# Kernel optimization log

Hardware: AMD Instinct MI355X
Metric: run time of the kernel (lower is better)

## Reference

```python
import jax, jax.numpy as jnp
import numpy as np

ATTN = 512
HIDDEN = 1024
NUM_GENES = 2048
NUM_GF = 4


def setup_inputs() -> dict:
    key = jax.random.key(0)
    ks = jax.random.split(key, 8)
    s = 0.1
    return {
        "genes": jax.random.normal(ks[0], (32, NUM_GENES, NUM_GF), dtype=jnp.float32),
        "smiles": jax.random.normal(ks[1], (32, 2048, HIDDEN), dtype=jnp.float32),
        "w_num_gene_features": s * jax.random.normal(ks[2], (NUM_GF,), dtype=jnp.float32),
        "w_genes": s * jax.random.normal(ks[3], (NUM_GENES, ATTN), dtype=jnp.float32),
        "b_genes": s * jax.random.normal(ks[4], (ATTN,), dtype=jnp.float32),
        "w_smiles": s * jax.random.normal(ks[5], (HIDDEN, ATTN), dtype=jnp.float32),
        "b_smiles": s * jax.random.normal(ks[6], (ATTN,), dtype=jnp.float32),
        "v": s * jax.random.normal(ks[7], (ATTN,), dtype=jnp.float32),
    }


def reference(genes, smiles, w_num_gene_features, w_genes, b_genes, w_smiles, b_smiles, v):
    # genes: [B, G, F] -> collapse feature axis: [B, G]
    genes_collapsed = jnp.einsum("bgf,f->bg", genes, w_num_gene_features)
    # gene context projection: [B, A]
    x = jnp.einsum("bg,ga->ba", genes_collapsed, w_genes) + b_genes
    # smiles projection: [B, T, A]
    y = jnp.einsum("bth,ha->bta", smiles, w_smiles) + b_smiles
    h = jnp.tanh(x[:, None, :] + y)  # [B, T, A]
    scores = jnp.einsum("bta,a->bt", h, v)  # [B, T]
    alphas = jax.nn.softmax(scores, axis=-1)  # [B, T]
    # attention-weighted sum over sequence: [B, H]
    return jnp.einsum("bth,bt->bh", smiles, alphas)
```

## Files before the change

kernel.cpp:

```cpp
#include <hip/hip_runtime.h>


typedef __bf16 bf16_t;
typedef bf16_t bf16x8 __attribute__((ext_vector_type(8)));
typedef float f32x4 __attribute__((ext_vector_type(4)));

__device__ __forceinline__ unsigned short f32_to_bf16_rne(float f) {
    unsigned int u = __builtin_bit_cast(unsigned int, f);
    u = (u + 0x7FFFu + ((u >> 16) & 1u)) >> 16;
    return (unsigned short)u;
}

__device__ __forceinline__ float fast_tanh(float x) {
    float cx = fminf(fmaxf(x, -30.f), 30.f);
    float e = __expf(2.f * cx);
    return (e - 1.f) / (e + 1.f);
}

__global__ void k0b_pack(const float* __restrict__ w, unsigned short* __restrict__ Bp) {
    int bid  = blockIdx.x;
    int lane = threadIdx.x;
    int atile = bid >> 5, gks = bid & 31;
    int col = atile * 16 + (lane & 15);
    int k0  = gks * 32 + (lane >> 4) * 8;
    unsigned short us[8];
#pragma unroll
    for (int e = 0; e < 8; ++e)
        us[e] = f32_to_bf16_rne(w[(size_t)(k0 + e) * 512 + col]);
    *(uint4*)(Bp + (size_t)bid * 512 + lane * 8) = *(const uint4*)us;
}

__global__ void k1a_gc(const float4* __restrict__ genes, const float* __restrict__ wngf,
                       float* __restrict__ gc) {
    int i = blockIdx.x * 256 + threadIdx.x;
    float4 g = genes[i];
    gc[i] = g.x * wngf[0] + g.y * wngf[1] + g.z * wngf[2] + g.w * wngf[3];
}

__global__ void k1b_x(const float* __restrict__ gc, const float* __restrict__ wg,
                      float* __restrict__ x) {
    __shared__ float gcl[256];
    int bx = blockIdx.x;
    int b = bx >> 4, ah = (bx >> 3) & 1, gch = bx & 7;
    int g0 = gch * 256;
    gcl[threadIdx.x] = gc[b * 2048 + g0 + threadIdx.x];
    __syncthreads();
    int a = ah * 256 + threadIdx.x;
    float s = 0.f;
#pragma unroll 8
    for (int g = 0; g < 256; ++g) s += gcl[g] * wg[(size_t)(g0 + g) * 512 + a];
    atomicAdd(&x[b * 512 + a], s);
}

__global__ __launch_bounds__(512, 4) void k2_scores(
    const float* __restrict__ smiles,
    const unsigned short* __restrict__ Bp,
    const float* __restrict__ xraw,
    const float* __restrict__ b_genes,
    const float* __restrict__ b_smiles,
    const float* __restrict__ v,
    float* __restrict__ scores)
{
    __shared__ unsigned short A_lds[2 * 64 * 128];
    __shared__ float score_lds[64];
    const int tid  = threadIdx.x;
    const int wave = tid >> 6;
    const int lane = tid & 63;
    const int l15  = lane & 15;
    const int l4   = lane >> 4;
    const int gm0  = blockIdx.x * 64;
    const int bidx = gm0 >> 11;
    const int wbase = wave * 64;

    const unsigned short* bpp = Bp + (size_t)(wave * 128) * 512 + lane * 8;

    const int srow = tid >> 3;
    const float* sptr = smiles + (size_t)(gm0 + srow) * 1024 + (tid & 7) * 16;
    const int sswz = (srow & 7) << 4;
    char* wr0 = (char*)A_lds + srow * 256 + (((tid & 7) * 32) ^ sswz);
    char* wr1 = (char*)A_lds + srow * 256 + ((((tid & 7) * 32) + 16) ^ sswz);

    if (tid < 64) score_lds[tid] = 0.f;

    float4 st0, st1, st2, st3;

    const f32x4 zero4 = {0.f, 0.f, 0.f, 0.f};
    f32x4 acc[4][4];
#pragma unroll
    for (int mt = 0; mt < 4; ++mt)
#pragma unroll
        for (int nt = 0; nt < 4; ++nt)
            acc[mt][nt] = zero4;

#define LOADREGS(kt)                                   \
    {   const float* p = sptr + (kt) * 128;            \
        st0 = *(const float4*)(p);                     \
        st1 = *(const float4*)(p + 4);                 \
        st2 = *(const float4*)(p + 8);                 \
        st3 = *(const float4*)(p + 12); }

#define CONVWRITE(buf)                                                     \
    {   union { unsigned short us[8]; uint4 u4; } pa, pb;                  \
        pa.us[0] = f32_to_bf16_rne(st0.x); pa.us[1] = f32_to_bf16_rne(st0.y); \
        pa.us[2] = f32_to_bf16_rne(st0.z); pa.us[3] = f32_to_bf16_rne(st0.w); \
        pa.us[4] = f32_to_bf16_rne(st1.x); pa.us[5] = f32_to_bf16_rne(st1.y); \
        pa.us[6] = f32_to_bf16_rne(st1.z); pa.us[7] = f32_to_bf16_rne(st1.w); \
        pb.us[0] = f32_to_bf16_rne(st2.x); pb.us[1] = f32_to_bf16_rne(st2.y); \
        pb.us[2] = f32_to_bf16_rne(st2.z); pb.us[3] = f32_to_bf16_rne(st2.w); \
        pb.us[4] = f32_to_bf16_rne(st3.x); pb.us[5] = f32_to_bf16_rne(st3.y); \
        pb.us[6] = f32_to_bf16_rne(st3.z); pb.us[7] = f32_to_bf16_rne(st3.w); \
        *(uint4*)(wr0 + (buf) * 16384) = pa.u4;                            \
        *(uint4*)(wr1 + (buf) * 16384) = pb.u4; }

#define COMPUTE(cur, kt)                                                      \
    _Pragma("unroll")                                                         \
    for (int ks4 = 0; ks4 < 4; ++ks4) {                                       \
        int gks = (kt) * 4 + ks4;                                             \
        bf16x8 af[4], bfb[4];                                                 \
        _Pragma("unroll")                                                     \
        for (int nt = 0; nt < 4; ++nt)                                        \
            bfb[nt] = *(const bf16x8*)(bpp + (nt * 32 + gks) * 512);          \
        _Pragma("unroll")                                                     \
        for (int mt = 0; mt < 4; ++mt) {                                      \
            int row = mt * 16 + l15;                                          \
            int byteoff = (cur) * 16384 + row * 256 +                         \
                          ((ks4 * 64 + l4 * 16) ^ ((row & 7) << 4));          \
            af[mt] = *(const bf16x8*)((const char*)A_lds + byteoff);          \
        }                                                                     \
        __builtin_amdgcn_s_setprio(1);                                        \
        _Pragma("unroll")                                                     \
        for (int mt = 0; mt < 4; ++mt)                                        \
            _Pragma("unroll")                                                 \
            for (int nt = 0; nt < 4; ++nt)                                    \
                acc[mt][nt] = __builtin_amdgcn_mfma_f32_16x16x32_bf16(        \
                    af[mt], bfb[nt], acc[mt][nt], 0, 0, 0);                   \
        __builtin_amdgcn_s_setprio(0);                                        \
    }

    LOADREGS(0);
    CONVWRITE(0);
    __syncthreads();

    int cur = 0;
#pragma unroll 1
    for (int kt = 0; kt < 7; ++kt) {
        LOADREGS(kt + 1);
        COMPUTE(cur, kt);
        CONVWRITE(cur ^ 1);
        __syncthreads();
        cur ^= 1;
    }
    COMPUTE(cur, 7);

#undef LOADREGS
#undef CONVWRITE
#undef COMPUTE

    float xbv[4], vv[4];
#pragma unroll
    for (int nt = 0; nt < 4; ++nt) {
        int a = wbase + nt * 16 + l15;
        xbv[nt] = xraw[bidx * 512 + a] + b_genes[a] + b_smiles[a];
        vv[nt]  = v[a];
    }
    float rs[4][4];
#pragma unroll
    for (int mt = 0; mt < 4; ++mt)
#pragma unroll
        for (int r = 0; r < 4; ++r)
            rs[mt][r] = 0.f;
#pragma unroll
    for (int mt = 0; mt < 4; ++mt)
#pragma unroll
        for (int nt = 0; nt < 4; ++nt)
#pragma unroll
            for (int r = 0; r < 4; ++r)
                rs[mt][r] += vv[nt] * fast_tanh(acc[mt][nt][r] + xbv[nt]);
#pragma unroll
    for (int mt = 0; mt < 4; ++mt)
#pragma unroll
        for (int r = 0; r < 4; ++r) {
            float s = rs[mt][r];
            s += __shfl_xor(s, 1);
            s += __shfl_xor(s, 2);
            s += __shfl_xor(s, 4);
            s += __shfl_xor(s, 8);
            rs[mt][r] = s;
        }
    if (l15 == 0) {
#pragma unroll
        for (int mt = 0; mt < 4; ++mt)
#pragma unroll
            for (int r = 0; r < 4; ++r)
                atomicAdd(&score_lds[mt * 16 + l4 * 4 + r], rs[mt][r]);
    }
    __syncthreads();
    if (tid < 64) scores[gm0 + tid] = score_lds[tid];
}

__global__ void k4_soft(const float* __restrict__ smiles,
                        const float* __restrict__ scores,
                        float* __restrict__ out)
{
    __shared__ float redmax[4], redsum[4], al_lds[64];
    int bx = blockIdx.x;
    int b  = bx >> 5;
    int tc = bx & 31;
    int tid = threadIdx.x;
    int wid = tid >> 6;

    float sv[8];
    float mx = -1e30f;
#pragma unroll
    for (int i = 0; i < 8; ++i) {
        sv[i] = scores[b * 2048 + i * 256 + tid];
        mx = fmaxf(mx, sv[i]);
    }
#pragma unroll
    for (int m = 32; m >= 1; m >>= 1) mx = fmaxf(mx, __shfl_xor(mx, m));
    if ((tid & 63) == 0) redmax[wid] = mx;
    __syncthreads();
    mx = fmaxf(fmaxf(redmax[0], redmax[1]), fmaxf(redmax[2], redmax[3]));
    float zp = 0.f;
#pragma unroll
    for (int i = 0; i < 8; ++i) zp += __expf(sv[i] - mx);
#pragma unroll
    for (int m = 32; m >= 1; m >>= 1) zp += __shfl_xor(zp, m);
    if ((tid & 63) == 0) redsum[wid] = zp;
    __syncthreads();
    float invZ = 1.f / (redsum[0] + redsum[1] + redsum[2] + redsum[3]);
    if (tid < 64)
        al_lds[tid] = __expf(scores[b * 2048 + tc * 64 + tid] - mx) * invZ;
    __syncthreads();

    int h = tid * 4;
    const float* sb = smiles + ((size_t)b * 2048 + tc * 64) * 1024;
    float4 acc = {0.f, 0.f, 0.f, 0.f};
#pragma unroll 4
    for (int t = 0; t < 64; ++t) {
        float a = al_lds[t];
        float4 sv4 = *(const float4*)(sb + (size_t)t * 1024 + h);
        acc.x += a * sv4.x;
        acc.y += a * sv4.y;
        acc.z += a * sv4.z;
        acc.w += a * sv4.w;
    }
    float* o = out + b * 1024 + h;
    atomicAdd(o + 0, acc.x);
    atomicAdd(o + 1, acc.y);
    atomicAdd(o + 2, acc.z);
    atomicAdd(o + 3, acc.w);
}

extern "C" void kernel_launch(void* const* d_in, const int* in_sizes, int n_in,
                              void* d_out, int out_size, void* d_ws, size_t ws_size,
                              hipStream_t stream) {
    const float* genes    = (const float*)d_in[0];
    const float* smiles   = (const float*)d_in[1];
    const float* w_ngf    = (const float*)d_in[2];
    const float* w_genes  = (const float*)d_in[3];
    const float* b_genes  = (const float*)d_in[4];
    const float* w_smiles = (const float*)d_in[5];
    const float* b_smiles = (const float*)d_in[6];
    const float* v        = (const float*)d_in[7];
    float* out = (float*)d_out;

    char* ws = (char*)d_ws;
    unsigned short* Bp = (unsigned short*)(ws);
    float* gc     = (float*)(ws + (1 << 20));
    float* x      = (float*)(ws + (1 << 20) + (256 << 10));
    float* scores = (float*)(ws + (1 << 20) + (320 << 10));

    hipMemsetAsync(out, 0, (size_t)32 * 1024 * sizeof(float), stream);
    hipMemsetAsync(x, 0, (size_t)64 * 1024, stream);

    k0b_pack<<<1024, 64, 0, stream>>>(w_smiles, Bp);
    k1a_gc<<<256, 256, 0, stream>>>((const float4*)genes, w_ngf, gc);
    k1b_x<<<512, 256, 0, stream>>>(gc, w_genes, x);
    k2_scores<<<1024, 512, 0, stream>>>(smiles, Bp, x, b_genes, b_smiles, v, scores);
    k4_soft<<<1024, 256, 0, stream>>>(smiles, scores, out);
}
```

Before: 163.8 us.

## Stage fp16 copy of smiles in scores kernel for cheaper weighted-sum pass

While the scores kernel streams smiles from memory, it also writes an fp16 copy to workspace. The softmax/weighted-sum kernel then reads that half-size copy instead of the fp32 smiles, cutting its read traffic in half. The cost is an extra 128 MB of writes in the scores kernel, added register and store pressure there, and lower precision in the output sum. The path runs only if the workspace is large enough.

```diff
diff --git a/kernel.cpp b/kernel.cpp
--- a/kernel.cpp
+++ b/kernel.cpp
@@ -15,6 +15,11 @@
     float cx = fminf(fmaxf(x, -30.f), 30.f);
     float e = __expf(2.f * cx);
     return (e - 1.f) / (e + 1.f);
+}
+
+__device__ __forceinline__ float f16b2f(unsigned short v) {
+    _Float16 h = __builtin_bit_cast(_Float16, v);
+    return (float)h;
 }
 
 __global__ void k0b_pack(const float* __restrict__ w, unsigned short* __restrict__ Bp) {
@@ -59,7 +64,8 @@
     const float* __restrict__ b_genes,
     const float* __restrict__ b_smiles,
     const float* __restrict__ v,
-    float* __restrict__ scores)
+    float* __restrict__ scores,
+    unsigned short* __restrict__ s16)
 {
     __shared__ unsigned short A_lds[2 * 64 * 128];
     __shared__ float score_lds[64];
@@ -76,6 +82,8 @@
 
     const int srow = tid >> 3;
     const float* sptr = smiles + (size_t)(gm0 + srow) * 1024 + (tid & 7) * 16;
+    unsigned short* s16p = s16 ? s16 + (size_t)(gm0 + srow) * 1024 + (tid & 7) * 16
+                               : (unsigned short*)0;
     const int sswz = (srow & 7) << 4;
     char* wr0 = (char*)A_lds + srow * 256 + (((tid & 7) * 32) ^ sswz);
     char* wr1 = (char*)A_lds + srow * 256 + ((((tid & 7) * 32) + 16) ^ sswz);
@@ -111,6 +119,21 @@
         pb.us[6] = f32_to_bf16_rne(st3.z); pb.us[7] = f32_to_bf16_rne(st3.w); \
         *(uint4*)(wr0 + (buf) * 16384) = pa.u4;                            \
         *(uint4*)(wr1 + (buf) * 16384) = pb.u4; }
+
+#define STORE16(kt)                                                           \
+    if (s16) {                                                                \
+        union { _Float16 h[8]; uint4 u4; } pf0, pf1;                          \
+        pf0.h[0] = (_Float16)st0.x; pf0.h[1] = (_Float16)st0.y;               \
+        pf0.h[2] = (_Float16)st0.z; pf0.h[3] = (_Float16)st0.w;               \
+        pf0.h[4] = (_Float16)st1.x; pf0.h[5] = (_Float16)st1.y;               \
+        pf0.h[6] = (_Float16)st1.z; pf0.h[7] = (_Float16)st1.w;               \
+        pf1.h[0] = (_Float16)st2.x; pf1.h[1] = (_Float16)st2.y;               \
+        pf1.h[2] = (_Float16)st2.z; pf1.h[3] = (_Float16)st2.w;               \
+        pf1.h[4] = (_Float16)st3.x; pf1.h[5] = (_Float16)st3.y;               \
+        pf1.h[6] = (_Float16)st3.z; pf1.h[7] = (_Float16)st3.w;               \
+        *(uint4*)(s16p + (kt) * 128)     = pf0.u4;                            \
+        *(uint4*)(s16p + (kt) * 128 + 8) = pf1.u4;                            \
+    }
 
 #define COMPUTE(cur, kt)                                                      \
     _Pragma("unroll")                                                         \
@@ -139,6 +162,7 @@
 
     LOADREGS(0);
     CONVWRITE(0);
+    STORE16(0);
     __syncthreads();
 
     int cur = 0;
@@ -147,6 +171,7 @@
         LOADREGS(kt + 1);
         COMPUTE(cur, kt);
         CONVWRITE(cur ^ 1);
+        STORE16(kt + 1);
         __syncthreads();
         cur ^= 1;
     }
@@ -154,6 +179,7 @@
 
 #undef LOADREGS
 #undef CONVWRITE
+#undef STORE16
 #undef COMPUTE
 
     float xbv[4], vv[4];
@@ -196,6 +222,60 @@
     }
     __syncthreads();
     if (tid < 64) scores[gm0 + tid] = score_lds[tid];
+}
+
+__global__ void k4_soft16(const unsigned short* __restrict__ s16,
+                          const float* __restrict__ scores,
+                          float* __restrict__ out)
+{
+    __shared__ float redmax[4], redsum[4], al_lds[64];
+    int bx = blockIdx.x;
+    int b  = bx >> 5;
+    int tc = bx & 31;
+    int tid = threadIdx.x;
+    int wid = tid >> 6;
+
+    float sv[8];
+    float mx = -1e30f;
+#pragma unroll
+    for (int i = 0; i < 8; ++i) {
+        sv[i] = scores[b * 2048 + i * 256 + tid];
+        mx = fmaxf(mx, sv[i]);
+    }
+#pragma unroll
+    for (int m = 32; m >= 1; m >>= 1) mx = fmaxf(mx, __shfl_xor(mx, m));
+    if ((tid & 63) == 0) redmax[wid] = mx;
+    __syncthreads();
+    mx = fmaxf(fmaxf(redmax[0], redmax[1]), fmaxf(redmax[2], redmax[3]));
+    float zp = 0.f;
+#pragma unroll
+    for (int i = 0; i < 8; ++i) zp += __expf(sv[i] - mx);
+#pragma unroll
+    for (int m = 32; m >= 1; m >>= 1) zp += __shfl_xor(zp, m);
+    if ((tid & 63) == 0) redsum[wid] = zp;
+    __syncthreads();
+    float invZ = 1.f / (redsum[0] + redsum[1] + redsum[2] + redsum[3]);
+    if (tid < 64)
+        al_lds[tid] = __expf(scores[b * 2048 + tc * 64 + tid] - mx) * invZ;
+    __syncthreads();
+
+    int h = tid * 4;
+    const unsigned short* sb = s16 + ((size_t)b * 2048 + tc * 64) * 1024;
+    float4 acc = {0.f, 0.f, 0.f, 0.f};
+#pragma unroll 4
+    for (int t = 0; t < 64; ++t) {
+        float a = al_lds[t];
+        ushort4 u = *(const ushort4*)(sb + (size_t)t * 1024 + h);
+        acc.x += a * f16b2f(u.x);
+        acc.y += a * f16b2f(u.y);
+        acc.z += a * f16b2f(u.z);
+        acc.w += a * f16b2f(u.w);
+    }
+    float* o = out + b * 1024 + h;
+    atomicAdd(o + 0, acc.x);
+    atomicAdd(o + 1, acc.y);
+    atomicAdd(o + 2, acc.z);
+    atomicAdd(o + 3, acc.w);
 }
 
 __global__ void k4_soft(const float* __restrict__ smiles,
@@ -271,12 +351,21 @@
     float* x      = (float*)(ws + (1 << 20) + (256 << 10));
     float* scores = (float*)(ws + (1 << 20) + (320 << 10));
 
+    const size_t s16_off   = (size_t)2 << 20;
+    const size_t s16_bytes = (size_t)32 * 2048 * 1024 * 2;
+    bool use16 = ws_size >= s16_off + s16_bytes;
+    unsigned short* s16 = use16 ? (unsigned short*)(ws + s16_off) : (unsigned short*)0;
+
     hipMemsetAsync(out, 0, (size_t)32 * 1024 * sizeof(float), stream);
     hipMemsetAsync(x, 0, (size_t)64 * 1024, stream);
 
     k0b_pack<<<1024, 64, 0, stream>>>(w_smiles, Bp);
     k1a_gc<<<256, 256, 0, stream>>>((const float4*)genes, w_ngf, gc);
     k1b_x<<<512, 256, 0, stream>>>(gc, w_genes, x);
-    k2_scores<<<1024, 512, 0, stream>>>(smiles, Bp, x, b_genes, b_smiles, v, scores);
-    k4_soft<<<1024, 256, 0, stream>>>(smiles, scores, out);
-}
+    k2_scores<<<1024, 512, 0, stream>>>(smiles, Bp, x, b_genes, b_smiles, v,
+                                        scores, s16);
+    if (use16)
+        k4_soft16<<<1024, 256, 0, stream>>>(s16, scores, out);
+    else
+        k4_soft<<<1024, 256, 0, stream>>>(smiles, scores, out);
+}
```

Result: slower. 186.9 us (+14.1%).

## Stage weight tiles in LDS via global_load_lds with 128-row, 1024-thread blocks

Applied to the files above, without the earlier changes.

The scores GEMM kernel now processes 128 sequence rows per block using 16 waves in a 2x8 grid. The packed bf16 weight tiles are staged into double-buffered LDS with direct global-to-LDS loads instead of being read by every wave from global memory. The K loop uses 32-wide steps, 32 iterations in all, with a new XOR swizzle for the A tile. This increases weight reuse across waves and halves the number of blocks. In exchange it needs about 80 KB of LDS per block and a barrier on every short K step, which may limit occupancy and add synchronisation overhead.

```diff
diff --git a/kernel.cpp b/kernel.cpp
--- a/kernel.cpp
+++ b/kernel.cpp
@@ -15,6 +15,15 @@
     float cx = fminf(fmaxf(x, -30.f), 30.f);
     float e = __expf(2.f * cx);
     return (e - 1.f) / (e + 1.f);
+}
+
+#define GLL16(g, l)                                                        \
+    __builtin_amdgcn_global_load_lds(                                      \
+        (const __attribute__((address_space(1))) void*)(g),                \
+        (__attribute__((address_space(3))) void*)(l), 16, 0, 0)
+
+__device__ __forceinline__ int swzg(int ff, int g) {
+    return (g & 56) | ((g ^ (g >> 3) ^ ff) & 7);
 }
 
 __global__ void k0b_pack(const float* __restrict__ w, unsigned short* __restrict__ Bp) {
@@ -52,7 +61,7 @@
     atomicAdd(&x[b * 512 + a], s);
 }
 
-__global__ __launch_bounds__(512, 4) void k2_scores(
+__global__ __launch_bounds__(1024, 4) void k2_scores(
     const float* __restrict__ smiles,
     const unsigned short* __restrict__ Bp,
     const float* __restrict__ xraw,
@@ -61,71 +70,63 @@
     const float* __restrict__ v,
     float* __restrict__ scores)
 {
-    __shared__ unsigned short A_lds[2 * 64 * 128];
-    __shared__ float score_lds[64];
+    __shared__ char LDS[81920];
+    char* const Aq0 = LDS;
+    char* const Aq1 = LDS + 8192;
+    char* const Bq0 = LDS + 16384;
+    char* const Bq1 = LDS + 49152;
+
     const int tid  = threadIdx.x;
     const int wave = tid >> 6;
     const int lane = tid & 63;
     const int l15  = lane & 15;
     const int l4   = lane >> 4;
-    const int gm0  = blockIdx.x * 64;
+    const int wr   = wave >> 3;
+    const int wc   = wave & 7;
+    const int gm0  = blockIdx.x * 128;
     const int bidx = gm0 >> 11;
-    const int wbase = wave * 64;
-
-    const unsigned short* bpp = Bp + (size_t)(wave * 128) * 512 + lane * 8;
 
     const int srow = tid >> 3;
-    const float* sptr = smiles + (size_t)(gm0 + srow) * 1024 + (tid & 7) * 16;
-    const int sswz = (srow & 7) << 4;
-    char* wr0 = (char*)A_lds + srow * 256 + (((tid & 7) * 32) ^ sswz);
-    char* wr1 = (char*)A_lds + srow * 256 + ((((tid & 7) * 32) + 16) ^ sswz);
-
-    if (tid < 64) score_lds[tid] = 0.f;
-
-    float4 st0, st1, st2, st3;
-
-    const f32x4 zero4 = {0.f, 0.f, 0.f, 0.f};
+    const int kq   = tid & 7;
+    const float* sptr = smiles + (size_t)(gm0 + srow) * 1024 + kq * 4;
+    const int aff  = srow >> 4;
+    const int ag   = (srow & 15) + 16 * (kq >> 1);
+    const int awoff = aff * 1024 + swzg(aff, ag) * 16 + (kq & 1) * 8;
+
+    float4 st;
     f32x4 acc[4][4];
 #pragma unroll
     for (int mt = 0; mt < 4; ++mt)
 #pragma unroll
         for (int nt = 0; nt < 4; ++nt)
-            acc[mt][nt] = zero4;
-
-#define LOADREGS(kt)                                   \
-    {   const float* p = sptr + (kt) * 128;            \
-        st0 = *(const float4*)(p);                     \
-        st1 = *(const float4*)(p + 4);                 \
-        st2 = *(const float4*)(p + 8);                 \
-        st3 = *(const float4*)(p + 12); }
-
-#define CONVWRITE(buf)                                                     \
-    {   union { unsigned short us[8]; uint4 u4; } pa, pb;                  \
-        pa.us[0] = f32_to_bf16_rne(st0.x); pa.us[1] = f32_to_bf16_rne(st0.y); \
-        pa.us[2] = f32_to_bf16_rne(st0.z); pa.us[3] = f32_to_bf16_rne(st0.w); \
-        pa.us[4] = f32_to_bf16_rne(st1.x); pa.us[5] = f32_to_bf16_rne(st1.y); \
-        pa.us[6] = f32_to_bf16_rne(st1.z); pa.us[7] = f32_to_bf16_rne(st1.w); \
-        pb.us[0] = f32_to_bf16_rne(st2.x); pb.us[1] = f32_to_bf16_rne(st2.y); \
-        pb.us[2] = f32_to_bf16_rne(st2.z); pb.us[3] = f32_to_bf16_rne(st2.w); \
-        pb.us[4] = f32_to_bf16_rne(st3.x); pb.us[5] = f32_to_bf16_rne(st3.y); \
-        pb.us[6] = f32_to_bf16_rne(st3.z); pb.us[7] = f32_to_bf16_rne(st3.w); \
-        *(uint4*)(wr0 + (buf) * 16384) = pa.u4;                            \
-        *(uint4*)(wr1 + (buf) * 16384) = pb.u4; }
-
-#define COMPUTE(cur, kt)                                                      \
+            acc[mt][nt] = f32x4{0.f, 0.f, 0.f, 0.f};
+
+#define LOADA(kt)  { st = *(const float4*)(sptr + (kt) * 32); }
+
+#define GLLB(kt, bq)                                                          \
     _Pragma("unroll")                                                         \
-    for (int ks4 = 0; ks4 < 4; ++ks4) {                                       \
-        int gks = (kt) * 4 + ks4;                                             \
-        bf16x8 af[4], bfb[4];                                                 \
+    for (int i = 0; i < 2; ++i) {                                             \
+        int atile = wave * 2 + i;                                             \
+        const char* g = (const char*)Bp +                                     \
+            (((size_t)atile * 32 + (kt)) << 10) + lane * 16;                  \
+        GLL16(g, (bq) + atile * 1024);                                        \
+    }
+
+#define CONVWRITE(aq)                                                         \
+    {   union { unsigned short us[4]; uint2 u2; } p;                          \
+        p.us[0] = f32_to_bf16_rne(st.x); p.us[1] = f32_to_bf16_rne(st.y);     \
+        p.us[2] = f32_to_bf16_rne(st.z); p.us[3] = f32_to_bf16_rne(st.w);     \
+        *(uint2*)((aq) + awoff) = p.u2; }
+
+#define COMPUTE(aq, bq)                                                       \
+    {   bf16x8 af[4], bfb[4];                                                 \
         _Pragma("unroll")                                                     \
         for (int nt = 0; nt < 4; ++nt)                                        \
-            bfb[nt] = *(const bf16x8*)(bpp + (nt * 32 + gks) * 512);          \
+            bfb[nt] = *(const bf16x8*)((bq) + (wc * 4 + nt) * 1024 + lane * 16); \
         _Pragma("unroll")                                                     \
         for (int mt = 0; mt < 4; ++mt) {                                      \
-            int row = mt * 16 + l15;                                          \
-            int byteoff = (cur) * 16384 + row * 256 +                         \
-                          ((ks4 * 64 + l4 * 16) ^ ((row & 7) << 4));          \
-            af[mt] = *(const bf16x8*)((const char*)A_lds + byteoff);          \
+            int ff = wr * 4 + mt;                                             \
+            af[mt] = *(const bf16x8*)((aq) + ff * 1024 + swzg(ff, lane) * 16); \
         }                                                                     \
         __builtin_amdgcn_s_setprio(1);                                        \
         _Pragma("unroll")                                                     \
@@ -137,65 +138,65 @@
         __builtin_amdgcn_s_setprio(0);                                        \
     }
 
-    LOADREGS(0);
-    CONVWRITE(0);
-    __syncthreads();
-
-    int cur = 0;
+    LOADA(0);
+    GLLB(0, Bq0);
+    CONVWRITE(Aq0);
+    __syncthreads();
+
 #pragma unroll 1
-    for (int kt = 0; kt < 7; ++kt) {
-        LOADREGS(kt + 1);
-        COMPUTE(cur, kt);
-        CONVWRITE(cur ^ 1);
+    for (int kt = 0; kt < 32; ++kt) {
+        char* aqc = (kt & 1) ? Aq1 : Aq0;
+        char* bqc = (kt & 1) ? Bq1 : Bq0;
+        char* aqn = (kt & 1) ? Aq0 : Aq1;
+        char* bqn = (kt & 1) ? Bq0 : Bq1;
+        if (kt < 31) {
+            LOADA(kt + 1);
+            GLLB(kt + 1, bqn);
+        }
+        COMPUTE(aqc, bqc);
+        if (kt < 31) CONVWRITE(aqn);
         __syncthreads();
-        cur ^= 1;
-    }
-    COMPUTE(cur, 7);
-
-#undef LOADREGS
+    }
+
+#undef LOADA
+#undef GLLB
 #undef CONVWRITE
 #undef COMPUTE
 
+    float* score_f = (float*)LDS;
+    if (tid < 128) score_f[tid] = 0.f;
+    __syncthreads();
+
     float xbv[4], vv[4];
 #pragma unroll
     for (int nt = 0; nt < 4; ++nt) {
-        int a = wbase + nt * 16 + l15;
+        int a = wc * 64 + nt * 16 + l15;
         xbv[nt] = xraw[bidx * 512 + a] + b_genes[a] + b_smiles[a];
         vv[nt]  = v[a];
     }
-    float rs[4][4];
-#pragma unroll
-    for (int mt = 0; mt < 4; ++mt)
-#pragma unroll
-        for (int r = 0; r < 4; ++r)
-            rs[mt][r] = 0.f;
-#pragma unroll
-    for (int mt = 0; mt < 4; ++mt)
+#pragma unroll
+    for (int mt = 0; mt < 4; ++mt) {
+        float rs[4];
+#pragma unroll
+        for (int r = 0; r < 4; ++r) rs[r] = 0.f;
 #pragma unroll
         for (int nt = 0; nt < 4; ++nt)
 #pragma unroll
             for (int r = 0; r < 4; ++r)
-                rs[mt][r] += vv[nt] * fast_tanh(acc[mt][nt][r] + xbv[nt]);
-#pragma unroll
-    for (int mt = 0; mt < 4; ++mt)
+                rs[r] += vv[nt] * fast_tanh(acc[mt][nt][r] + xbv[nt]);
 #pragma unroll
         for (int r = 0; r < 4; ++r) {
-            float s = rs[mt][r];
+            float s = rs[r];
             s += __shfl_xor(s, 1);
             s += __shfl_xor(s, 2);
             s += __shfl_xor(s, 4);
             s += __shfl_xor(s, 8);
-            rs[mt][r] = s;
+            if (l15 == 0)
+                atomicAdd(&score_f[wr * 64 + mt * 16 + l4 * 4 + r], s);
         }
-    if (l15 == 0) {
-#pragma unroll
-        for (int mt = 0; mt < 4; ++mt)
-#pragma unroll
-            for (int r = 0; r < 4; ++r)
-                atomicAdd(&score_lds[mt * 16 + l4 * 4 + r], rs[mt][r]);
-    }
-    __syncthreads();
-    if (tid < 64) scores[gm0 + tid] = score_lds[tid];
+    }
+    __syncthreads();
+    if (tid < 128) scores[gm0 + tid] = score_f[tid];
 }
 
 __global__ void k4_soft(const float* __restrict__ smiles,
@@ -277,6 +278,6 @@
     k0b_pack<<<1024, 64, 0, stream>>>(w_smiles, Bp);
     k1a_gc<<<256, 256, 0, stream>>>((const float4*)genes, w_ngf, gc);
     k1b_x<<<512, 256, 0, stream>>>(gc, w_genes, x);
-    k2_scores<<<1024, 512, 0, stream>>>(smiles, Bp, x, b_genes, b_smiles, v, scores);
+    k2_scores<<<512, 1024, 0, stream>>>(smiles, Bp, x, b_genes, b_smiles, v, scores);
     k4_soft<<<1024, 256, 0, stream>>>(smiles, scores, out);
 }
```

Measured after the change: 171.3 us. 1.05x slower.
